# Kernel optimization log

Hardware: AMD Instinct MI355X
Metric: run time of the kernel (lower is better)

The kernel has to match this reference:

```python
import jax, jax.numpy as jnp
import numpy as np

B, T, NLAT, N, D = 8, 4, 64, 2048, 1024
HEADS, HEAD_DIM = 16, 64
ADIM = HEADS * HEAD_DIM
EPS = 1e-5


def layer_norm(x, w, b):
    mu = jnp.mean(x, axis=-1, keepdims=True)
    var = jnp.var(x, axis=-1, keepdims=True)
    return (x - mu) * jax.lax.rsqrt(var + EPS) * w + b


def setup_inputs() -> dict:
    key = jax.random.key(0)
    ks = jax.random.split(key, 8)
    s = 0.02
    return {
        "latents": jax.random.normal(ks[0], (B, T, NLAT, D), jnp.float32),
        "x": jax.random.normal(ks[1], (B, T, N, D), jnp.float32),
        "Wq": jax.random.normal(ks[2], (D, ADIM), jnp.float32) * s,     # [in, out]
        "Wkv": jax.random.normal(ks[3], (D, 2 * ADIM), jnp.float32) * s,
        "Wout": jax.random.normal(ks[4], (ADIM, D), jnp.float32) * s,
        "bout": jnp.zeros((D,), jnp.float32),
        "lnl_w": jnp.ones((D,), jnp.float32),
        "lnl_b": jnp.zeros((D,), jnp.float32),
        "lnm_w": jnp.ones((D,), jnp.float32),
        "lnm_b": jnp.zeros((D,), jnp.float32),
    }


def reference(latents, x, Wq, Wkv, Wout, bout, lnl_w, lnl_b, lnm_w, lnm_b):
    scale = HEAD_DIM ** (-0.5)
    lat = layer_norm(latents, lnl_w, lnl_b)          # [B,T,NLAT,D]
    med = layer_norm(x, lnm_w, lnm_b)                # [B,T,N,D]
    q = lat @ Wq                                      # [B,T,NLAT,ADIM]
    kv_in = jnp.concatenate((med, lat), axis=-2)      # [B,T,N+NLAT,D]
    kv = kv_in @ Wkv                                  # [B,T,N+NLAT,2*ADIM]
    k, v = jnp.split(kv, 2, axis=-1)
    # split heads: b t n (h d) -> b h t n d
    def split_heads(z):
        b, t, n, _ = z.shape
        return z.reshape(b, t, n, HEADS, HEAD_DIM).transpose(0, 3, 1, 2, 4)
    q = split_heads(q) * scale
    k = split_heads(k)
    v = split_heads(v)
    scores = jnp.einsum('bhtid,bhtjd->bhtij', q, k)   # [B,H,T,NLAT,N+NLAT]
    attn = jax.nn.softmax(scores, axis=-1)            # max-subtract handled internally
    out = jnp.einsum('bhtij,bhtjd->bhtid', attn, v)   # [B,H,T,NLAT,HEAD_DIM]
    out = out.transpose(0, 2, 3, 1, 4).reshape(B, T, NLAT, ADIM)
    return out @ Wout + bout
```

## Files before the change

### kernel.cpp

```cpp
#include <hip/hip_runtime.h>
#include <hip/hip_bf16.h>
#include <stdint.h>

#define B_    8
#define T_    4
#define NLAT  64
#define NMED  2048
#define NKV   2112
#define D_    1024
#define HEADS 16
#define HD    64
#define ADIM  1024
#define BT    32

#define GK    1024
#define GN    2048
#define GM    67584
#define MT2   264
#define NSLC  32

typedef __attribute__((ext_vector_type(8))) short bf16x8;
typedef __attribute__((ext_vector_type(4))) float f32x4;

__device__ __forceinline__ ushort f2bf(float f) {
  union { float f; uint32_t u; } v; v.f = f;
  return (ushort)((v.u + 0x7fff + ((v.u >> 16) & 1)) >> 16);
}

__device__ __forceinline__ void gload_lds16(const void* g, void* l) {
  __builtin_amdgcn_global_load_lds(
      (const __attribute__((address_space(1))) void*)g,
      (__attribute__((address_space(3))) void*)l, 16, 0, 0);
}

__device__ __forceinline__ f32x4 mfma16(bf16x8 a, bf16x8 b, f32x4 c) {
  return __builtin_amdgcn_mfma_f32_16x16x32_bf16(a, b, c, 0, 0, 0);
}

__global__ __launch_bounds__(256) void wtrans(const float* __restrict__ src,
                                              ushort* __restrict__ dst,
                                              int K, int Nm) {
  __shared__ float t[64][65];
  const int tr = blockIdx.y, tc = blockIdx.x;
  const int c = threadIdx.x & 63;
  const int r4 = threadIdx.x >> 6;
#pragma unroll
  for (int rr = 0; rr < 16; ++rr) {
    int r = r4 + rr * 4;
    t[r][c] = src[(size_t)(tr * 64 + r) * Nm + tc * 64 + c];
  }
  __syncthreads();
#pragma unroll
  for (int rr = 0; rr < 16; ++rr) {
    int n = r4 + rr * 4;
    dst[(size_t)(tc * 64 + n) * K + tr * 64 + c] = f2bf(t[c][n]);
  }
}

__global__ __launch_bounds__(256) void ln_kernel(
    const float* __restrict__ lat, const float* __restrict__ x,
    const float* __restrict__ lnl_w, const float* __restrict__ lnl_b,
    const float* __restrict__ lnm_w, const float* __restrict__ lnm_b,
    ushort* __restrict__ kvin) {
  const int row = blockIdx.x;
  const int bt = row / NKV;
  const int j = row - bt * NKV;
  const float* src;
  const float* w;
  const float* bb;
  if (j < NMED) {
    src = x + ((size_t)bt * NMED + j) * D_;
    w = lnm_w; bb = lnm_b;
  } else {
    src = lat + ((size_t)bt * NLAT + (j - NMED)) * D_;
    w = lnl_w; bb = lnl_b;
  }
  const int tid = threadIdx.x;
  float4 v = ((const float4*)src)[tid];
  float s = v.x + v.y + v.z + v.w;
  float s2 = v.x * v.x + v.y * v.y + v.z * v.z + v.w * v.w;
#pragma unroll
  for (int off = 1; off < 64; off <<= 1) {
    s += __shfl_xor(s, off, 64);
    s2 += __shfl_xor(s2, off, 64);
  }
  __shared__ float red[8];
  const int wave = tid >> 6;
  if ((tid & 63) == 0) { red[wave] = s; red[4 + wave] = s2; }
  __syncthreads();
  float S = red[0] + red[1] + red[2] + red[3];
  float S2 = red[4] + red[5] + red[6] + red[7];
  const float inv = 1.f / (float)D_;
  float mu = S * inv;
  float var = S2 * inv - mu * mu;
  float rs = rsqrtf(var + 1e-5f);
  float4 wv = ((const float4*)w)[tid];
  float4 bv = ((const float4*)bb)[tid];
  ushort4 ov;
  ov.x = f2bf((v.x - mu) * rs * wv.x + bv.x);
  ov.y = f2bf((v.y - mu) * rs * wv.y + bv.y);
  ov.z = f2bf((v.z - mu) * rs * wv.z + bv.z);
  ov.w = f2bf((v.w - mu) * rs * wv.w + bv.w);
  ((ushort4*)(kvin + (size_t)row * D_))[tid] = ov;
}

template <int AMODE, int OUTMODE>
__global__ __launch_bounds__(256) void gemm_bt(const ushort* __restrict__ A,
                                               const ushort* __restrict__ Bt,
                                               void* __restrict__ C,
                                               const float* __restrict__ bias,
                                               int M, int N, int K, int ldc) {
  __shared__ ushort lsA[128 * 32];
  __shared__ ushort lsB[128 * 32];
  const int tid = threadIdx.x;
  const int lane = tid & 63;
  const int wave = tid >> 6;
  const int brow = blockIdx.y * 128;
  const int bcol = blockIdx.x * 128;
  const int wr = (wave >> 1) * 64;
  const int wc = (wave & 1) * 64;
  const int lr = lane & 15;
  const int lk = (lane >> 4) * 8;

  f32x4 acc[4][4];
#pragma unroll
  for (int m = 0; m < 4; ++m)
#pragma unroll
    for (int n = 0; n < 4; ++n) acc[m][n] = (f32x4){0.f, 0.f, 0.f, 0.f};

  const int wbase = (tid & 192) * 16;

  for (int k0 = 0; k0 < K; k0 += 32) {
#pragma unroll
    for (int i = 0; i < 2; ++i) {
      int idx = i * 256 + tid;
      int r = idx >> 2;
      int cc = (idx & 3) * 8;
      long arow;
      if (AMODE == 1) {
        int gr = brow + r;
        arow = (long)(gr >> 6) * NKV + NMED + (gr & 63);
      } else {
        arow = brow + r;
      }
      gload_lds16(A + arow * (long)K + k0 + cc, (char*)lsA + i * 4096 + wbase);
      gload_lds16(Bt + (long)(bcol + r) * K + k0 + cc, (char*)lsB + i * 4096 + wbase);
    }
    __syncthreads();

    bf16x8 af[4], bf[4];
#pragma unroll
    for (int m = 0; m < 4; ++m)
      af[m] = *(const bf16x8*)&lsA[(wr + m * 16 + lr) * 32 + lk];
#pragma unroll
    for (int n = 0; n < 4; ++n)
      bf[n] = *(const bf16x8*)&lsB[(wc + n * 16 + lr) * 32 + lk];
#pragma unroll
    for (int m = 0; m < 4; ++m)
#pragma unroll
      for (int n = 0; n < 4; ++n) acc[m][n] = mfma16(af[m], bf[n], acc[m][n]);
    __syncthreads();
  }

#pragma unroll
  for (int m = 0; m < 4; ++m) {
#pragma unroll
    for (int n = 0; n < 4; ++n) {
      int row0 = brow + wr + m * 16 + (lane >> 4) * 4;
      int col = bcol + wc + n * 16 + lr;
#pragma unroll
      for (int r = 0; r < 4; ++r) {
        long off = (long)(row0 + r) * ldc + col;
        float v = acc[m][n][r];
        if (OUTMODE == 1) ((ushort*)C)[off] = f2bf(v * 0.125f);
        else ((float*)C)[off] = v + bias[col];
      }
    }
  }
}

__global__ __launch_bounds__(512, 2) void gemm256(const ushort* __restrict__ A,
                                                  const ushort* __restrict__ Bt,
                                                  ushort* __restrict__ C) {
  extern __shared__ __align__(16) char smem[];
  const int tid = threadIdx.x;
  const int lane = tid & 63;
  const int wv = tid >> 6;
  const int wm = wv >> 2;
  const int wn = wv & 3;
  const int lr = lane & 15;
  const int lg = lane >> 4;

  const int g = blockIdx.x;
  const int v = (g & 7) * MT2 + (g >> 3);
  const int bx = v & 7;
  const int by = v >> 3;
  const long brow = (long)by * 256;
  const int bcol = bx * 256;

  const int pcx = lg ^ ((lr >> 1) & 3);

  f32x4 acc[8][4];
#pragma unroll
  for (int m = 0; m < 8; ++m)
#pragma unroll
    for (int n = 0; n < 4; ++n) acc[m][n] = (f32x4){0.f, 0.f, 0.f, 0.f};

  const int s0 = tid, s1 = 512 + tid;
  const int r0 = s0 >> 2, r1 = s1 >> 2;
  const int c0 = (s0 & 3) ^ ((s0 >> 3) & 3);
  const int c1 = (s1 & 3) ^ ((s1 >> 3) & 3);
  const int o0 = (s0 & ~63) * 16;
  const int o1 = (s1 & ~63) * 16;

#define STAGE_A(slc, slot)                                                     \
  {                                                                            \
    long k0 = (long)(slc) * 32;                                                \
    char* db = smem + (slot) * 32768;                                          \
    gload_lds16(A + (brow + r0) * (long)GK + k0 + c0 * 8, db + o0);            \
    gload_lds16(A + (brow + r1) * (long)GK + k0 + c1 * 8, db + o1);            \
  }
#define STAGE_B(slc, slot)                                                     \
  {                                                                            \
    long k0 = (long)(slc) * 32;                                                \
    char* db = smem + (slot) * 32768 + 16384;                                  \
    gload_lds16(Bt + (long)(bcol + r0) * GK + k0 + c0 * 8, db + o0);           \
    gload_lds16(Bt + (long)(bcol + r1) * GK + k0 + c1 * 8, db + o1);           \
  }

  STAGE_A(0, 0); STAGE_B(0, 0);
  STAGE_A(1, 1); STAGE_B(1, 1);
  STAGE_A(2, 2); STAGE_B(2, 2);
  asm volatile("s_waitcnt vmcnt(8)" ::: "memory");
  __builtin_amdgcn_s_barrier();
  __builtin_amdgcn_sched_barrier(0);

  for (int t = 0; t < NSLC; ++t) {
    const char* sA = smem + (t & 3) * 32768;
    const char* sB = sA + 16384;
    const int ts = (t + 3 < NSLC) ? t + 3 : t;
    const int wslot = (t + 3) & 3;
    bf16x8 af[4], bf[4];

#pragma unroll
    for (int m = 0; m < 4; ++m) {
      int row = wm * 128 + m * 16 + lr;
      af[m] = *(const bf16x8*)(sA + row * 64 + pcx * 16);
    }
#pragma unroll
    for (int n = 0; n < 4; ++n) {
      int row = wn * 64 + n * 16 + lr;
      bf[n] = *(const bf16x8*)(sB + row * 64 + pcx * 16);
    }
    STAGE_A(ts, wslot);
    __builtin_amdgcn_s_barrier();
    asm volatile("s_waitcnt lgkmcnt(0)" ::: "memory");
    __builtin_amdgcn_sched_barrier(0);
    __builtin_amdgcn_s_setprio(1);
#pragma unroll
    for (int m = 0; m < 4; ++m)
#pragma unroll
      for (int n = 0; n < 4; ++n)
        acc[m][n] = mfma16(bf[n], af[m], acc[m][n]);
    __builtin_amdgcn_s_setprio(0);
    __builtin_amdgcn_sched_barrier(0);
    __builtin_amdgcn_s_barrier();

#pragma unroll
    for (int m = 0; m < 4; ++m) {
      int row = wm * 128 + (m + 4) * 16 + lr;
      af[m] = *(const bf16x8*)(sA + row * 64 + pcx * 16);
    }
    STAGE_B(ts, wslot);
    asm volatile("s_waitcnt vmcnt(8)" ::: "memory");
    __builtin_amdgcn_s_barrier();
    asm volatile("s_waitcnt lgkmcnt(0)" ::: "memory");
    __builtin_amdgcn_sched_barrier(0);
    __builtin_amdgcn_s_setprio(1);
#pragma unroll
    for (int m = 0; m < 4; ++m)
#pragma unroll
      for (int n = 0; n < 4; ++n)
        acc[m + 4][n] = mfma16(bf[n], af[m], acc[m + 4][n]);
    __builtin_amdgcn_s_setprio(0);
    __builtin_amdgcn_sched_barrier(0);
    __builtin_amdgcn_s_barrier();
  }
#undef STAGE_A
#undef STAGE_B

#pragma unroll
  for (int m = 0; m < 8; ++m) {
    long row = brow + wm * 128 + m * 16 + lr;
    ushort* crow = C + row * GN + bcol + wn * 64 + lg * 4;
#pragma unroll
    for (int n = 0; n < 4; ++n) {
      ushort4 o;
      o.x = f2bf(acc[m][n][0]);
      o.y = f2bf(acc[m][n][1]);
      o.z = f2bf(acc[m][n][2]);
      o.w = f2bf(acc[m][n][3]);
      *(ushort4*)(crow + n * 16) = o;
    }
  }
}

__global__ __launch_bounds__(256) void attn_kernel(const ushort* __restrict__ q,
                                                   const ushort* __restrict__ kv,
                                                   ushort* __restrict__ o) {
  const int blk = blockIdx.x;
  const int bt = blk >> 4;
  const int h = blk & 15;
  const int tid = threadIdx.x;
  const int wave = tid >> 6;
  const int lane = tid & 63;
  const int lr = lane & 15;
  const int lg = lane >> 4;

  __shared__ ushort vt[64][72];
  __shared__ ushort pl[4][16][72];

  const ushort* qbase = q + (size_t)(bt * 64 + wave * 16) * ADIM + h * HD;
  bf16x8 qf[2];
#pragma unroll
  for (int ks = 0; ks < 2; ++ks)
    qf[ks] = *(const bf16x8*)(qbase + (size_t)lr * ADIM + ks * 32 + lg * 8);

  const ushort* kvb = kv + (size_t)bt * NKV * 2048;

  f32x4 accO[4];
#pragma unroll
  for (int n = 0; n < 4; ++n) accO[n] = (f32x4){0.f, 0.f, 0.f, 0.f};
  float mrun[4] = {-1e30f, -1e30f, -1e30f, -1e30f};
  float lrun[4] = {0.f, 0.f, 0.f, 0.f};

  for (int jt = 0; jt < NKV / 64; ++jt) {
    const int j0 = jt * 64;
    __syncthreads();

    {
      int jj = tid >> 2;
      int dbase = (tid & 3) * 16;
#pragma unroll
      for (int half = 0; half < 2; ++half) {
        int d0 = dbase + half * 8;
        bf16x8 vv = *(const bf16x8*)(kvb + (size_t)(j0 + jj) * 2048 + ADIM + h * HD + d0);
#pragma unroll
        for (int e = 0; e < 8; ++e) vt[d0 + e][jj] = ((const ushort*)&vv)[e];
      }
    }

    f32x4 s[4];
#pragma unroll
    for (int nj = 0; nj < 4; ++nj) s[nj] = (f32x4){0.f, 0.f, 0.f, 0.f};
#pragma unroll
    for (int nj = 0; nj < 4; ++nj)
#pragma unroll
      for (int ks = 0; ks < 2; ++ks) {
        bf16x8 kf = *(const bf16x8*)(kvb + (size_t)(j0 + nj * 16 + lr) * 2048 +
                                     h * HD + ks * 32 + lg * 8);
        s[nj] = mfma16(qf[ks], kf, s[nj]);
      }

    float mt[4], corr[4], psum[4];
#pragma unroll
    for (int r = 0; r < 4; ++r)
      mt[r] = fmaxf(fmaxf(s[0][r], s[1][r]), fmaxf(s[2][r], s[3][r]));
#pragma unroll
    for (int off = 1; off < 16; off <<= 1)
#pragma unroll
      for (int r = 0; r < 4; ++r) mt[r] = fmaxf(mt[r], __shfl_xor(mt[r], off, 64));
#pragma unroll
    for (int r = 0; r < 4; ++r) {
      float mn = fmaxf(mrun[r], mt[r]);
      corr[r] = __expf(mrun[r] - mn);
      mrun[r] = mn;
      psum[r] = 0.f;
    }
#pragma unroll
    for (int nj = 0; nj < 4; ++nj)
#pragma unroll
      for (int r = 0; r < 4; ++r) {
        float pv = __expf(s[nj][r] - mrun[r]);
        s[nj][r] = pv;
        psum[r] += pv;
      }
#pragma unroll
    for (int off = 1; off < 16; off <<= 1)
#pragma unroll
      for (int r = 0; r < 4; ++r) psum[r] += __shfl_xor(psum[r], off, 64);
#pragma unroll
    for (int r = 0; r < 4; ++r) lrun[r] = lrun[r] * corr[r] + psum[r];
#pragma unroll
    for (int n = 0; n < 4; ++n)
#pragma unroll
      for (int r = 0; r < 4; ++r) accO[n][r] *= corr[r];

#pragma unroll
    for (int nj = 0; nj < 4; ++nj)
#pragma unroll
      for (int r = 0; r < 4; ++r)
        pl[wave][lg * 4 + r][nj * 16 + lr] = f2bf(s[nj][r]);
    __syncthreads();

    bf16x8 pf[2];
#pragma unroll
    for (int ks = 0; ks < 2; ++ks)
      pf[ks] = *(const bf16x8*)&pl[wave][lr][ks * 32 + lg * 8];
#pragma unroll
    for (int nd = 0; nd < 4; ++nd)
#pragma unroll
      for (int ks = 0; ks < 2; ++ks) {
        bf16x8 vf = *(const bf16x8*)&vt[nd * 16 + lr][ks * 32 + lg * 8];
        accO[nd] = mfma16(pf[ks], vf, accO[nd]);
      }
  }

#pragma unroll
  for (int nd = 0; nd < 4; ++nd)
#pragma unroll
    for (int r = 0; r < 4; ++r) {
      float vv = accO[nd][r] / lrun[r];
      int row = bt * 64 + wave * 16 + lg * 4 + r;
      o[(size_t)row * ADIM + h * HD + nd * 16 + lr] = f2bf(vv);
    }
}

extern "C" void kernel_launch(void* const* d_in, const int* in_sizes, int n_in,
                              void* d_out, int out_size, void* d_ws, size_t ws_size,
                              hipStream_t stream) {
  const float* latents = (const float*)d_in[0];
  const float* x = (const float*)d_in[1];
  const float* Wq = (const float*)d_in[2];
  const float* Wkv = (const float*)d_in[3];
  const float* Wout = (const float*)d_in[4];
  const float* bout = (const float*)d_in[5];
  const float* lnl_w = (const float*)d_in[6];
  const float* lnl_b = (const float*)d_in[7];
  const float* lnm_w = (const float*)d_in[8];
  const float* lnm_b = (const float*)d_in[9];

  char* ws = (char*)d_ws;
  size_t off = 0;
  auto alloc = [&](size_t bytes) -> void* {
    void* p = ws + off;
    off += (bytes + 255) & ~(size_t)255;
    return p;
  };
  ushort* kvin = (ushort*)alloc((size_t)BT * NKV * D_ * 2);
  ushort* kvo  = (ushort*)alloc((size_t)BT * NKV * 2048 * 2);
  ushort* qb   = (ushort*)alloc((size_t)BT * NLAT * ADIM * 2);
  ushort* ao   = (ushort*)alloc((size_t)BT * NLAT * ADIM * 2);
  ushort* WqT  = (ushort*)alloc((size_t)D_ * ADIM * 2);
  ushort* WkvT = (ushort*)alloc((size_t)D_ * 2 * ADIM * 2);
  ushort* WoutT = (ushort*)alloc((size_t)ADIM * D_ * 2);

  hipFuncSetAttribute((const void*)gemm256,
                      hipFuncAttributeMaxDynamicSharedMemorySize, 131072);

  wtrans<<<dim3(ADIM / 64, D_ / 64), 256, 0, stream>>>(Wq, WqT, D_, ADIM);
  wtrans<<<dim3(2 * ADIM / 64, D_ / 64), 256, 0, stream>>>(Wkv, WkvT, D_, 2 * ADIM);
  wtrans<<<dim3(D_ / 64, ADIM / 64), 256, 0, stream>>>(Wout, WoutT, ADIM, D_);

  ln_kernel<<<BT * NKV, 256, 0, stream>>>(latents, x, lnl_w, lnl_b, lnm_w, lnm_b, kvin);

  gemm_bt<1, 1><<<dim3(ADIM / 128, BT * NLAT / 128), 256, 0, stream>>>(
      kvin, WqT, qb, nullptr, BT * NLAT, ADIM, D_, ADIM);

  gemm256<<<dim3(MT2 * 8), 512, 131072, stream>>>(kvin, WkvT, kvo);

  attn_kernel<<<BT * HEADS, 256, 0, stream>>>(qb, kvo, ao);

  gemm_bt<0, 2><<<dim3(D_ / 128, BT * NLAT / 128), 256, 0, stream>>>(
      ao, WoutT, d_out, bout, BT * NLAT, D_, ADIM, D_);
}
```

Before: 601.1 us.

## Double-buffer LDS fragment registers to overlap next-slice reads with MFMA

Restructures the GEMM main loop so the A and B register fragments for the next K-slice are read from LDS while the current slice's second half of MFMAs runs. B fragments ping-pong between two register sets, with the loop unrolled by two, and partial lgkmcnt waits replace full drains. The aim is to hide LDS read latency behind matrix instructions, at the cost of more VGPRs, which may reduce occupancy or cause spills.

New measurement: 596.6 us. About the same (-0.7%).

```diff
diff --git a/kernel.cpp b/kernel.cpp
--- a/kernel.cpp
+++ b/kernel.cpp
@@ -199,6 +199,8 @@
   const int bcol = bx * 256;
 
   const int pcx = lg ^ ((lr >> 1) & 3);
+  const int rbA = wm * 128 + lr;
+  const int rbB = wn * 64 + lr;
 
   f32x4 acc[8][4];
 #pragma unroll
@@ -228,64 +230,80 @@
     gload_lds16(Bt + (long)(bcol + r1) * GK + k0 + c1 * 8, db + o1);           \
   }
 
+  bf16x8 a0[4], a1[4], b0[4], b1[4];
+
   STAGE_A(0, 0); STAGE_B(0, 0);
   STAGE_A(1, 1); STAGE_B(1, 1);
   STAGE_A(2, 2); STAGE_B(2, 2);
   asm volatile("s_waitcnt vmcnt(8)" ::: "memory");
   __builtin_amdgcn_s_barrier();
+#pragma unroll
+  for (int m = 0; m < 4; ++m)
+    a0[m] = *(const bf16x8*)(smem + (rbA + m * 16) * 64 + pcx * 16);
+#pragma unroll
+  for (int n = 0; n < 4; ++n)
+    b0[n] = *(const bf16x8*)(smem + 16384 + (rbB + n * 16) * 64 + pcx * 16);
   __builtin_amdgcn_sched_barrier(0);
 
-  for (int t = 0; t < NSLC; ++t) {
-    const char* sA = smem + (t & 3) * 32768;
-    const char* sB = sA + 16384;
-    const int ts = (t + 3 < NSLC) ? t + 3 : t;
-    const int wslot = (t + 3) & 3;
-    bf16x8 af[4], bf[4];
-
-#pragma unroll
-    for (int m = 0; m < 4; ++m) {
-      int row = wm * 128 + m * 16 + lr;
-      af[m] = *(const bf16x8*)(sA + row * 64 + pcx * 16);
-    }
-#pragma unroll
-    for (int n = 0; n < 4; ++n) {
-      int row = wn * 64 + n * 16 + lr;
-      bf[n] = *(const bf16x8*)(sB + row * 64 + pcx * 16);
-    }
-    STAGE_A(ts, wslot);
-    __builtin_amdgcn_s_barrier();
-    asm volatile("s_waitcnt lgkmcnt(0)" ::: "memory");
-    __builtin_amdgcn_sched_barrier(0);
-    __builtin_amdgcn_s_setprio(1);
-#pragma unroll
-    for (int m = 0; m < 4; ++m)
-#pragma unroll
-      for (int n = 0; n < 4; ++n)
-        acc[m][n] = mfma16(bf[n], af[m], acc[m][n]);
-    __builtin_amdgcn_s_setprio(0);
-    __builtin_amdgcn_sched_barrier(0);
-    __builtin_amdgcn_s_barrier();
-
-#pragma unroll
-    for (int m = 0; m < 4; ++m) {
-      int row = wm * 128 + (m + 4) * 16 + lr;
-      af[m] = *(const bf16x8*)(sA + row * 64 + pcx * 16);
-    }
-    STAGE_B(ts, wslot);
-    asm volatile("s_waitcnt vmcnt(8)" ::: "memory");
-    __builtin_amdgcn_s_barrier();
-    asm volatile("s_waitcnt lgkmcnt(0)" ::: "memory");
-    __builtin_amdgcn_sched_barrier(0);
-    __builtin_amdgcn_s_setprio(1);
-#pragma unroll
-    for (int m = 0; m < 4; ++m)
-#pragma unroll
-      for (int n = 0; n < 4; ++n)
-        acc[m + 4][n] = mfma16(bf[n], af[m], acc[m + 4][n]);
-    __builtin_amdgcn_s_setprio(0);
-    __builtin_amdgcn_sched_barrier(0);
-    __builtin_amdgcn_s_barrier();
-  }
+#define SLICE(T, BCUR, BNXT)                                                   \
+  {                                                                            \
+    const int t_ = (T);                                                        \
+    const char* sA_ = smem + (t_ & 3) * 32768;                                 \
+    const int ts_ = (t_ + 3 < NSLC) ? t_ + 3 : t_;                             \
+    const int ws_ = (t_ + 3) & 3;                                              \
+                                                        \
+    _Pragma("unroll")                                                          \
+    for (int m = 0; m < 4; ++m)                                                \
+      a1[m] = *(const bf16x8*)(sA_ + (rbA + (m + 4) * 16) * 64 + pcx * 16);    \
+    STAGE_A(ts_, ws_);                                                         \
+    __builtin_amdgcn_sched_barrier(0);                                         \
+    __builtin_amdgcn_s_barrier();                                              \
+    asm volatile("s_waitcnt lgkmcnt(4)" ::: "memory");                         \
+    __builtin_amdgcn_sched_barrier(0);                                         \
+    __builtin_amdgcn_s_setprio(1);                                             \
+    _Pragma("unroll")                                                          \
+    for (int m = 0; m < 4; ++m)                                                \
+      _Pragma("unroll")                                                        \
+      for (int n = 0; n < 4; ++n)                                              \
+        acc[m][n] = mfma16(BCUR[n], a0[m], acc[m][n]);                         \
+    __builtin_amdgcn_s_setprio(0);                                             \
+    __builtin_amdgcn_sched_barrier(0);                                         \
+    __builtin_amdgcn_s_barrier();                                              \
+                                                        \
+    STAGE_B(ts_, ws_);                                                         \
+    asm volatile("s_waitcnt vmcnt(8)" ::: "memory");                           \
+    __builtin_amdgcn_sched_barrier(0);                                         \
+    __builtin_amdgcn_s_barrier();                                              \
+    {                                                                          \
+      const int tn_ = (t_ + 1 < NSLC) ? t_ + 1 : t_;                           \
+      const char* nA_ = smem + (tn_ & 3) * 32768;                              \
+      const char* nB_ = nA_ + 16384;                                           \
+      _Pragma("unroll")                                                        \
+      for (int m = 0; m < 4; ++m)                                              \
+        a0[m] = *(const bf16x8*)(nA_ + (rbA + m * 16) * 64 + pcx * 16);        \
+      _Pragma("unroll")                                                        \
+      for (int n = 0; n < 4; ++n)                                              \
+        BNXT[n] = *(const bf16x8*)(nB_ + (rbB + n * 16) * 64 + pcx * 16);      \
+    }                                                                          \
+    __builtin_amdgcn_sched_barrier(0);                                         \
+    asm volatile("s_waitcnt lgkmcnt(8)" ::: "memory");                         \
+    __builtin_amdgcn_sched_barrier(0);                                         \
+    __builtin_amdgcn_s_setprio(1);                                             \
+    _Pragma("unroll")                                                          \
+    for (int m = 0; m < 4; ++m)                                                \
+      _Pragma("unroll")                                                        \
+      for (int n = 0; n < 4; ++n)                                              \
+        acc[m + 4][n] = mfma16(BCUR[n], a1[m], acc[m + 4][n]);                 \
+    __builtin_amdgcn_s_setprio(0);                                             \
+    __builtin_amdgcn_sched_barrier(0);                                         \
+    __builtin_amdgcn_s_barrier();                                              \
+  }
+
+  for (int t = 0; t < NSLC; t += 2) {
+    SLICE(t, b0, b1);
+    SLICE(t + 1, b1, b0);
+  }
+#undef SLICE
 #undef STAGE_A
 #undef STAGE_B
 
```
